# Kernel tuning notes

Hardware: AMD Instinct MI355X
Metric: run time of the kernel (lower is better)

The kernel has to match this reference:

```python
import jax, jax.numpy as jnp
import numpy as np

N_HEAD = 12
N_TILES = 10  # forward hardcodes t = T // 10 and repeats the tril mask 10x10


def setup_inputs() -> dict:
    key = jax.random.key(0)
    ks = jax.random.split(key, 9)
    B, T, C = 2, 2560, 768
    s = 1.0 / np.sqrt(C)
    x = jax.random.normal(ks[0], (B, T, C), dtype=jnp.float32)
    Wk = jax.random.normal(ks[1], (C, C), dtype=jnp.float32) * s
    bk = jnp.zeros((C,), dtype=jnp.float32)
    Wq = jax.random.normal(ks[2], (C, C), dtype=jnp.float32) * s
    bq = jnp.zeros((C,), dtype=jnp.float32)
    Wv = jax.random.normal(ks[3], (C, C), dtype=jnp.float32) * s
    bv = jnp.zeros((C,), dtype=jnp.float32)
    Wp = jax.random.normal(ks[4], (C, C), dtype=jnp.float32) * s
    bp = jnp.zeros((C,), dtype=jnp.float32)
    return {"x": x, "Wk": Wk, "bk": bk, "Wq": Wq, "bq": bq,
            "Wv": Wv, "bv": bv, "Wp": Wp, "bp": bp}


def reference(x, Wk, bk, Wq, bq, Wv, bv, Wp, bp):
    B, T, C = x.shape
    hd = C // N_HEAD
    t = T // N_TILES
    # linear projections (torch nn.Linear: x @ W.T + b)
    k = (x @ Wk.T + bk).reshape(B, T, N_HEAD, hd).transpose(0, 2, 1, 3)  # [B,H,T,hd]
    q = (x @ Wq.T + bq).reshape(B, T, N_HEAD, hd).transpose(0, 2, 1, 3)
    v = (x @ Wv.T + bv).reshape(B, T, N_HEAD, hd).transpose(0, 2, 1, 3)
    att = jnp.einsum('bhqd,bhkd->bhqk', q, k) * (1.0 / np.sqrt(hd))  # [B,H,T,T]
    # repeated block-tril mask: tril(t,t) tiled 10x10 over TxT
    idx = jnp.arange(T)
    mask = (idx[:, None] % t) >= (idx[None, :] % t)  # [T,T] bool
    att = jnp.where(mask[None, None], att, -jnp.inf)
    att = jax.nn.softmax(att, axis=-1)
    y = jnp.einsum('bhqk,bhkd->bhqd', att, v)  # [B,H,T,hd]
    y = y.transpose(0, 2, 1, 3).reshape(B, T, C)
    return y @ Wp.T + bp
```

## Files before the change

### kernel.cpp

```cpp
#include <hip/hip_runtime.h>

typedef unsigned short u16;
typedef unsigned int u32;
typedef __bf16 bf16x8 __attribute__((ext_vector_type(8)));
typedef short s16x4 __attribute__((ext_vector_type(4)));
typedef float f32x4 __attribute__((ext_vector_type(4)));

#define CC 768
#define TT 2560
#define NH 12
#define HD 64
#define KDIM 768

#define QSCALE 0.18033688011112042f

__device__ __forceinline__ u16 f2bf(float f) {
  u32 u = __builtin_bit_cast(u32, f);
  u32 r = u + 0x7fffu + ((u >> 16) & 1u);
  return (u16)(r >> 16);
}

#if __has_builtin(__builtin_amdgcn_mfma_f32_16x16x16bf16_1k)
__device__ __forceinline__ f32x4 mfma16b(s16x4 a, s16x4 b, f32x4 c) {
  return __builtin_amdgcn_mfma_f32_16x16x16bf16_1k(a, b, c, 0, 0, 0);
}
#else
__device__ __forceinline__ f32x4 mfma16b(s16x4 a, s16x4 b, f32x4 c) {
  f32x4 d;
  asm("v_mfma_f32_16x16x16_bf16 %0, %1, %2, %3\n\ts_nop 7\n\ts_nop 7"
      : "=v"(d) : "v"(a), "v"(b), "v"(c));
  return d;
}
#endif

__global__ void convall(const float* __restrict__ x,
                        const float* __restrict__ Wq, const float* __restrict__ Wk,
                        const float* __restrict__ Wv, const float* __restrict__ Wp,
                        u16* __restrict__ xb, u16* __restrict__ wqb, u16* __restrict__ wkb,
                        u16* __restrict__ wvb, u16* __restrict__ wpb,
                        int nx4, int nw4) {
  int z = blockIdx.y;
  const float* in; u16* out; int n4;
  switch (z) {
    case 0: in = x;  out = xb;  n4 = nx4; break;
    case 1: in = Wq; out = wqb; n4 = nw4; break;
    case 2: in = Wk; out = wkb; n4 = nw4; break;
    case 3: in = Wv; out = wvb; n4 = nw4; break;
    default: in = Wp; out = wpb; n4 = nw4; break;
  }
  int i = blockIdx.x * blockDim.x + threadIdx.x;
  if (i >= n4) return;
  float4 v = ((const float4*)in)[i];
  ushort4 o;
  o.x = f2bf(v.x); o.y = f2bf(v.y); o.z = f2bf(v.z); o.w = f2bf(v.w);
  ((ushort4*)out)[i] = o;
}

__global__ __launch_bounds__(256) void gemm_qkv(
    const u16* __restrict__ xb,
    const u16* __restrict__ wqb, const u16* __restrict__ wkb, const u16* __restrict__ wvb,
    const float* __restrict__ bq, const float* __restrict__ bk, const float* __restrict__ bv,
    u16* __restrict__ qo, u16* __restrict__ ko, u16* __restrict__ vo)
{
  __shared__ __align__(16) u16 lds_a[128 * 72];
  __shared__ __align__(16) u16 lds_b[128 * 72];
  int z = blockIdx.z;
  const u16* W = (z == 0) ? wqb : (z == 1 ? wkb : wvb);
  const float* bias = (z == 0) ? bq : (z == 1 ? bk : bv);
  int n0 = blockIdx.x * 128;
  int m0 = blockIdx.y * 128;
  int tid = threadIdx.x;
  int lane = tid & 63, wv_ = tid >> 6;
  int wm = wv_ & 1, wn = wv_ >> 1;
  int mcol = lane & 15, quad = lane >> 4;
  int chunk = tid & 7, rbase = tid >> 3;

  f32x4 acc[4][4] = {};

  for (int k0 = 0; k0 < KDIM; k0 += 64) {
    __syncthreads();
#pragma unroll
    for (int r = 0; r < 4; ++r) {
      int row = rbase + r * 32;
      *(uint4*)&lds_a[row * 72 + chunk * 8] =
          *(const uint4*)&xb[(size_t)(m0 + row) * KDIM + k0 + chunk * 8];
      *(uint4*)&lds_b[row * 72 + chunk * 8] =
          *(const uint4*)&W[(size_t)(n0 + row) * KDIM + k0 + chunk * 8];
    }
    __syncthreads();
#pragma unroll
    for (int kc = 0; kc < 2; ++kc) {
      bf16x8 af[4], bfr[4];
#pragma unroll
      for (int i = 0; i < 4; i++)
        af[i] = *(const bf16x8*)&lds_a[(wm * 64 + i * 16 + mcol) * 72 + kc * 32 + quad * 8];
#pragma unroll
      for (int i = 0; i < 4; i++)
        bfr[i] = *(const bf16x8*)&lds_b[(wn * 64 + i * 16 + mcol) * 72 + kc * 32 + quad * 8];
      if (z == 2) {
#pragma unroll
        for (int i = 0; i < 4; i++)
#pragma unroll
          for (int j = 0; j < 4; j++)
            acc[i][j] = __builtin_amdgcn_mfma_f32_16x16x32_bf16(af[i], bfr[j], acc[i][j], 0, 0, 0);
      } else {
#pragma unroll
        for (int i = 0; i < 4; i++)
#pragma unroll
          for (int j = 0; j < 4; j++)
            acc[i][j] = __builtin_amdgcn_mfma_f32_16x16x32_bf16(bfr[j], af[i], acc[i][j], 0, 0, 0);
      }
    }
  }

  if (z == 2) {
#pragma unroll
    for (int i = 0; i < 4; i++) {
      int rowb = m0 + wm * 64 + i * 16 + quad * 4;
      int b = rowb / TT;
      int tt0 = rowb - b * TT;
#pragma unroll
      for (int j = 0; j < 4; j++) {
        int col = n0 + wn * 64 + j * 16 + mcol;
        int h = col >> 6, d = col & 63;
        float bb_ = bias[col];
        size_t bhoff = (size_t)(b * NH + h) * (TT * HD);
        ushort4 pk;
        pk.x = f2bf(acc[i][j][0] + bb_);
        pk.y = f2bf(acc[i][j][1] + bb_);
        pk.z = f2bf(acc[i][j][2] + bb_);
        pk.w = f2bf(acc[i][j][3] + bb_);
        *(ushort4*)&vo[bhoff + (size_t)(tt0 >> 4) * 1024 + d * 16 + (tt0 & 15)] = pk;
      }
    }
  } else {
    u16* dst = (z == 0) ? qo : ko;
    float scale = (z == 0) ? QSCALE : 1.0f;
#pragma unroll
    for (int i = 0; i < 4; i++) {
      int token = m0 + wm * 64 + i * 16 + mcol;
      int b = token / TT;
      int tt = token - b * TT;
#pragma unroll
      for (int j = 0; j < 4; j++) {
        int ch0 = n0 + wn * 64 + j * 16 + quad * 4;
        int h = ch0 >> 6, d4 = ch0 & 63;
        float4 bb4 = *(const float4*)&bias[ch0];
        size_t bhoff = (size_t)(b * NH + h) * (TT * HD);
        ushort4 pk;
        pk.x = f2bf((acc[i][j][0] + bb4.x) * scale);
        pk.y = f2bf((acc[i][j][1] + bb4.y) * scale);
        pk.z = f2bf((acc[i][j][2] + bb4.z) * scale);
        pk.w = f2bf((acc[i][j][3] + bb4.w) * scale);
        if (z == 0) {
          *(ushort4*)&dst[bhoff + (size_t)tt * HD + d4] = pk;
        } else {
          *(ushort4*)&dst[bhoff + (size_t)(tt >> 4) * 1024 + (d4 >> 5) * 512 +
                          (tt & 15) * 32 + (d4 & 31)] = pk;
        }
      }
    }
  }
}

struct Strip {
  bf16x8 qf0, qf1;
  f32x4 o0, o1, o2, o3;
  f32x4 racc;
};

__device__ __forceinline__ void strip_step(
    Strip& S, bf16x8 kf0, bf16x8 kf1,
    s16x4 vf0, s16x4 vf1, s16x4 vf2, s16x4 vf3,
    bool maskg, int mcol, int quad)
{
  f32x4 st = {0.f, 0.f, 0.f, 0.f};
  st = __builtin_amdgcn_mfma_f32_16x16x32_bf16(kf0, S.qf0, st, 0, 0, 0);
  st = __builtin_amdgcn_mfma_f32_16x16x32_bf16(kf1, S.qf1, st, 0, 0, 0);
  float p0 = __builtin_amdgcn_exp2f(st[0]);
  float p1 = __builtin_amdgcn_exp2f(st[1]);
  float p2 = __builtin_amdgcn_exp2f(st[2]);
  float p3 = __builtin_amdgcn_exp2f(st[3]);
  if (maskg) {
    int j0 = quad * 4;
    p0 = (j0 + 0 > mcol) ? 0.f : p0;
    p1 = (j0 + 1 > mcol) ? 0.f : p1;
    p2 = (j0 + 2 > mcol) ? 0.f : p2;
    p3 = (j0 + 3 > mcol) ? 0.f : p3;
  }
  uint2 pk;
  pk.x = __builtin_amdgcn_perm(__builtin_bit_cast(u32, p1),
                               __builtin_bit_cast(u32, p0), 0x07060302u);
  pk.y = __builtin_amdgcn_perm(__builtin_bit_cast(u32, p3),
                               __builtin_bit_cast(u32, p2), 0x07060302u);
  s16x4 pf = __builtin_bit_cast(s16x4, pk);
  const s16x4 ones = {0x3F80, 0x3F80, 0x3F80, 0x3F80};
  S.racc = mfma16b(ones, pf, S.racc);
  S.o0 = mfma16b(vf0, pf, S.o0);
  S.o1 = mfma16b(vf1, pf, S.o1);
  S.o2 = mfma16b(vf2, pf, S.o2);
  S.o3 = mfma16b(vf3, pf, S.o3);
}

#define OSTR 68

__global__ __launch_bounds__(128) void attn(
    const u16* __restrict__ q, const u16* __restrict__ kg,
    const u16* __restrict__ vg, u16* __restrict__ y)
{
  __shared__ float lds_o[4][16 * OSTR];
  __shared__ float lds_r[64];

  int tid = threadIdx.x;
  int lane = tid & 63, w = tid >> 6;
  int mcol = lane & 15, quad = lane >> 4;
  int gid = blockIdx.x;
  int c = gid & 7;
  int idx = gid >> 3;
  int sub = idx / 40;
  int s = idx - sub * 40;
  int bh = c * 3 + sub;
  int hb = s >> 3;
  int r = s & 7;
  int b = bh / NH, h = bh - b * NH;
  const u16* qp = q + (size_t)bh * TT * HD;
  const u16* kp = kg + (size_t)bh * TT * HD;
  const u16* vp = vg + (size_t)bh * TT * HD;

  int base = hb * 512;
  int rh = 7 - r;
  int qr[4];
  qr[0] = base + r * 16;
  qr[1] = base + 128 + rh * 16;
  qr[2] = base + 256 + r * 16;
  qr[3] = base + 384 + rh * 16;

  Strip S[4];
#pragma unroll
  for (int i = 0; i < 4; ++i) {
    S[i].qf0 = *(const bf16x8*)&qp[(size_t)(qr[i] + mcol) * HD + quad * 8];
    S[i].qf1 = *(const bf16x8*)&qp[(size_t)(qr[i] + mcol) * HD + 32 + quad * 8];
    S[i].o0 = {0.f, 0.f, 0.f, 0.f};
    S[i].o1 = {0.f, 0.f, 0.f, 0.f};
    S[i].o2 = {0.f, 0.f, 0.f, 0.f};
    S[i].o3 = {0.f, 0.f, 0.f, 0.f};
    S[i].racc = {0.f, 0.f, 0.f, 0.f};
  }

  int koff = mcol * 32 + quad * 8;
  int voff = mcol * 16 + quad * 4;

  for (int kt = w * 10; kt < w * 10 + 10; ++kt) {
    const u16* ktb = kp + kt * (128 * HD);
    const u16* vtb = vp + kt * (128 * HD);
    if ((kt & 1) == 0) {
#pragma unroll
      for (int g = 0; g < 8; ++g) {
        bf16x8 kf0 = *(const bf16x8*)&ktb[g * 1024 + koff];
        bf16x8 kf1 = *(const bf16x8*)&ktb[g * 1024 + 512 + koff];
        s16x4 vf0 = *(const s16x4*)&vtb[g * 1024 + 0 * 256 + voff];
        s16x4 vf1 = *(const s16x4*)&vtb[g * 1024 + 1 * 256 + voff];
        s16x4 vf2 = *(const s16x4*)&vtb[g * 1024 + 2 * 256 + voff];
        s16x4 vf3 = *(const s16x4*)&vtb[g * 1024 + 3 * 256 + voff];
        strip_step(S[1], kf0, kf1, vf0, vf1, vf2, vf3, false, mcol, quad);
        strip_step(S[3], kf0, kf1, vf0, vf1, vf2, vf3, false, mcol, quad);
        if (g <= r) {
          bool mg = (g == r);
          strip_step(S[0], kf0, kf1, vf0, vf1, vf2, vf3, mg, mcol, quad);
          strip_step(S[2], kf0, kf1, vf0, vf1, vf2, vf3, mg, mcol, quad);
        }
      }
    } else {
      for (int g = 0; g <= rh; ++g) {
        bf16x8 kf0 = *(const bf16x8*)&ktb[g * 1024 + koff];
        bf16x8 kf1 = *(const bf16x8*)&ktb[g * 1024 + 512 + koff];
        s16x4 vf0 = *(const s16x4*)&vtb[g * 1024 + 0 * 256 + voff];
        s16x4 vf1 = *(const s16x4*)&vtb[g * 1024 + 1 * 256 + voff];
        s16x4 vf2 = *(const s16x4*)&vtb[g * 1024 + 2 * 256 + voff];
        s16x4 vf3 = *(const s16x4*)&vtb[g * 1024 + 3 * 256 + voff];
        bool mg = (g == rh);
        strip_step(S[1], kf0, kf1, vf0, vf1, vf2, vf3, mg, mcol, quad);
        strip_step(S[3], kf0, kf1, vf0, vf1, vf2, vf3, mg, mcol, quad);
      }
    }
  }

  if (w == 1) {
#pragma unroll
    for (int i = 0; i < 4; ++i) {
      f32x4 oo[4] = {S[i].o0, S[i].o1, S[i].o2, S[i].o3};
#pragma unroll
      for (int df = 0; df < 4; ++df)
        *(f32x4*)&lds_o[i][mcol * OSTR + df * 16 + quad * 4] = oo[df];
      if (quad == 0) lds_r[i * 16 + mcol] = S[i].racc[0];
    }
  }
  __syncthreads();
  if (w == 0) {
#pragma unroll
    for (int i = 0; i < 4; ++i) {
      float denom = S[i].racc[0] + lds_r[i * 16 + mcol];
      float inv = 1.0f / denom;
      f32x4 oo[4] = {S[i].o0, S[i].o1, S[i].o2, S[i].o3};
      size_t yrow = ((size_t)(b * TT + qr[i] + mcol)) * CC + h * HD;
#pragma unroll
      for (int df = 0; df < 4; ++df) {
        f32x4 other = *(const f32x4*)&lds_o[i][mcol * OSTR + df * 16 + quad * 4];
        ushort4 pk;
        pk.x = f2bf((oo[df][0] + other[0]) * inv);
        pk.y = f2bf((oo[df][1] + other[1]) * inv);
        pk.z = f2bf((oo[df][2] + other[2]) * inv);
        pk.w = f2bf((oo[df][3] + other[3]) * inv);
        *(ushort4*)&y[yrow + df * 16 + quad * 4] = pk;
      }
    }
  }
}

__global__ __launch_bounds__(256) void gemm_out(
    const u16* __restrict__ yb, const u16* __restrict__ wpb,
    const float* __restrict__ bp, float* __restrict__ out)
{
  __shared__ __align__(16) u16 lds_a[64 * 72];
  __shared__ __align__(16) u16 lds_b[128 * 72];
  int n0 = blockIdx.x * 128;
  int m0 = blockIdx.y * 64;
  int tid = threadIdx.x;
  int lane = tid & 63, wv_ = tid >> 6;
  int wm = wv_ & 1, wn = wv_ >> 1;
  int mcol = lane & 15, quad = lane >> 4;
  int chunk = tid & 7, rbase = tid >> 3;

  f32x4 acc[2][4] = {};

  for (int k0 = 0; k0 < KDIM; k0 += 64) {
    __syncthreads();
#pragma unroll
    for (int r = 0; r < 2; ++r) {
      int row = rbase + r * 32;
      *(uint4*)&lds_a[row * 72 + chunk * 8] =
          *(const uint4*)&yb[(size_t)(m0 + row) * KDIM + k0 + chunk * 8];
    }
#pragma unroll
    for (int r = 0; r < 4; ++r) {
      int row = rbase + r * 32;
      *(uint4*)&lds_b[row * 72 + chunk * 8] =
          *(const uint4*)&wpb[(size_t)(n0 + row) * KDIM + k0 + chunk * 8];
    }
    __syncthreads();
#pragma unroll
    for (int kc = 0; kc < 2; ++kc) {
      bf16x8 af[2], bfr[4];
#pragma unroll
      for (int i = 0; i < 2; i++)
        af[i] = *(const bf16x8*)&lds_a[(wm * 32 + i * 16 + mcol) * 72 + kc * 32 + quad * 8];
#pragma unroll
      for (int j = 0; j < 4; j++)
        bfr[j] = *(const bf16x8*)&lds_b[(wn * 64 + j * 16 + mcol) * 72 + kc * 32 + quad * 8];
#pragma unroll
      for (int i = 0; i < 2; i++)
#pragma unroll
        for (int j = 0; j < 4; j++)
          acc[i][j] = __builtin_amdgcn_mfma_f32_16x16x32_bf16(bfr[j], af[i], acc[i][j], 0, 0, 0);
    }
  }

#pragma unroll
  for (int i = 0; i < 2; i++) {
    int token = m0 + wm * 32 + i * 16 + mcol;
#pragma unroll
    for (int j = 0; j < 4; j++) {
      int ch0 = n0 + wn * 64 + j * 16 + quad * 4;
      float4 bb4 = *(const float4*)&bp[ch0];
      float4 o4;
      o4.x = acc[i][j][0] + bb4.x;
      o4.y = acc[i][j][1] + bb4.y;
      o4.z = acc[i][j][2] + bb4.z;
      o4.w = acc[i][j][3] + bb4.w;
      *(float4*)&out[(size_t)token * CC + ch0] = o4;
    }
  }
}

extern "C" void kernel_launch(void* const* d_in, const int* in_sizes, int n_in,
                              void* d_out, int out_size, void* d_ws, size_t ws_size,
                              hipStream_t stream) {
  const float* x  = (const float*)d_in[0];
  const float* Wk = (const float*)d_in[1];
  const float* bk = (const float*)d_in[2];
  const float* Wq = (const float*)d_in[3];
  const float* bq = (const float*)d_in[4];
  const float* Wv = (const float*)d_in[5];
  const float* bv = (const float*)d_in[6];
  const float* Wp = (const float*)d_in[7];
  const float* bp = (const float*)d_in[8];
  float* out = (float*)d_out;

  char* ws = (char*)d_ws;
  size_t off = 0;
  auto alloc = [&](size_t bytes) {
    void* p = ws + off;
    off += (bytes + 255) & ~(size_t)255;
    return p;
  };
  const size_t NX = (size_t)2 * TT * CC;
  const size_t NW = (size_t)CC * CC;
  u16* xb  = (u16*)alloc(NX * 2);
  u16* wqb = (u16*)alloc(NW * 2);
  u16* wkb = (u16*)alloc(NW * 2);
  u16* wvb = (u16*)alloc(NW * 2);
  u16* wpb = (u16*)alloc(NW * 2);
  u16* qws = (u16*)alloc(NX * 2);
  u16* kws = (u16*)alloc(NX * 2);
  u16* vgw = (u16*)alloc(NX * 2);
  u16* yws = (u16*)alloc(NX * 2);

  int nx4 = (int)(NX / 4), nw4 = (int)(NW / 4);
  convall<<<dim3((nx4 + 255) / 256, 5), 256, 0, stream>>>(
      x, Wq, Wk, Wv, Wp, xb, wqb, wkb, wvb, wpb, nx4, nw4);

  gemm_qkv<<<dim3(6, 40, 3), 256, 0, stream>>>(xb, wqb, wkb, wvb, bq, bk, bv,
                                               qws, kws, vgw);
  attn<<<dim3(960), 128, 0, stream>>>(qws, kws, vgw, yws);
  gemm_out<<<dim3(6, 80), 256, 0, stream>>>(yws, wpb, bp, out);
}
```

Measured before the change: 188.9 us.

## Split attention key tiles across four waves with tree reduction

New measurement: 194.4 us. +2.9%, slower.

```diff
diff --git a/kernel.cpp b/kernel.cpp
--- a/kernel.cpp
+++ b/kernel.cpp
@@ -204,12 +204,12 @@
 
 #define OSTR 68
 
-__global__ __launch_bounds__(128) void attn(
+__global__ __launch_bounds__(256) void attn(
     const u16* __restrict__ q, const u16* __restrict__ kg,
     const u16* __restrict__ vg, u16* __restrict__ y)
 {
-  __shared__ float lds_o[4][16 * OSTR];
-  __shared__ float lds_r[64];
+  __shared__ float lds_o[2][4][16 * OSTR];
+  __shared__ float lds_r[2][64];
 
   int tid = threadIdx.x;
   int lane = tid & 63, w = tid >> 6;
@@ -250,7 +250,7 @@
   int koff = mcol * 32 + quad * 8;
   int voff = mcol * 16 + quad * 4;
 
-  for (int kt = w * 10; kt < w * 10 + 10; ++kt) {
+  for (int kt = w * 5; kt < w * 5 + 5; ++kt) {
     const u16* ktb = kp + kt * (128 * HD);
     const u16* vtb = vp + kt * (128 * HD);
     if ((kt & 1) == 0) {
@@ -285,35 +285,60 @@
     }
   }
 
-  if (w == 1) {
-#pragma unroll
-    for (int i = 0; i < 4; ++i) {
-      f32x4 oo[4] = {S[i].o0, S[i].o1, S[i].o2, S[i].o3};
-#pragma unroll
-      for (int df = 0; df < 4; ++df)
-        *(f32x4*)&lds_o[i][mcol * OSTR + df * 16 + quad * 4] = oo[df];
-      if (quad == 0) lds_r[i * 16 + mcol] = S[i].racc[0];
-    }
+  auto spillb = [&](const Strip& Si, int bi, int i) {
+    f32x4 oo[4] = {Si.o0, Si.o1, Si.o2, Si.o3};
+#pragma unroll
+    for (int df = 0; df < 4; ++df)
+      *(f32x4*)&lds_o[bi][i][mcol * OSTR + df * 16 + quad * 4] = oo[df];
+    if (quad == 0) lds_r[bi][i * 16 + mcol] = Si.racc[0];
+  };
+  auto gatherb = [&](Strip& Si, int bi, int i) {
+    f32x4 t0 = *(const f32x4*)&lds_o[bi][i][mcol * OSTR + 0 * 16 + quad * 4];
+    f32x4 t1 = *(const f32x4*)&lds_o[bi][i][mcol * OSTR + 1 * 16 + quad * 4];
+    f32x4 t2 = *(const f32x4*)&lds_o[bi][i][mcol * OSTR + 2 * 16 + quad * 4];
+    f32x4 t3 = *(const f32x4*)&lds_o[bi][i][mcol * OSTR + 3 * 16 + quad * 4];
+    Si.o0 += t0; Si.o1 += t1; Si.o2 += t2; Si.o3 += t3;
+    Si.racc[0] += lds_r[bi][i * 16 + mcol];
+  };
+  auto finish = [&](const Strip& Si, int i, int qrow) {
+    float denom = Si.racc[0] + lds_r[0][i * 16 + mcol];
+    float inv = 1.0f / denom;
+    f32x4 oo[4] = {Si.o0, Si.o1, Si.o2, Si.o3};
+    size_t yrow = ((size_t)(b * TT + qrow + mcol)) * CC + h * HD;
+#pragma unroll
+    for (int df = 0; df < 4; ++df) {
+      f32x4 other = *(const f32x4*)&lds_o[0][i][mcol * OSTR + df * 16 + quad * 4];
+      ushort4 pk;
+      pk.x = f2bf((oo[df][0] + other[0]) * inv);
+      pk.y = f2bf((oo[df][1] + other[1]) * inv);
+      pk.z = f2bf((oo[df][2] + other[2]) * inv);
+      pk.w = f2bf((oo[df][3] + other[3]) * inv);
+      *(ushort4*)&y[yrow + df * 16 + quad * 4] = pk;
+    }
+  };
+
+  if (w & 1) {
+    int bi = w >> 1;
+    spillb(S[0], bi, 0); spillb(S[1], bi, 1);
+    spillb(S[2], bi, 2); spillb(S[3], bi, 3);
+  }
+  __syncthreads();
+  if (!(w & 1)) {
+    int bi = w >> 1;
+    gatherb(S[0], bi, 0); gatherb(S[1], bi, 1);
+    gatherb(S[2], bi, 2); gatherb(S[3], bi, 3);
   }
   __syncthreads();
   if (w == 0) {
-#pragma unroll
-    for (int i = 0; i < 4; ++i) {
-      float denom = S[i].racc[0] + lds_r[i * 16 + mcol];
-      float inv = 1.0f / denom;
-      f32x4 oo[4] = {S[i].o0, S[i].o1, S[i].o2, S[i].o3};
-      size_t yrow = ((size_t)(b * TT + qr[i] + mcol)) * CC + h * HD;
-#pragma unroll
-      for (int df = 0; df < 4; ++df) {
-        f32x4 other = *(const f32x4*)&lds_o[i][mcol * OSTR + df * 16 + quad * 4];
-        ushort4 pk;
-        pk.x = f2bf((oo[df][0] + other[0]) * inv);
-        pk.y = f2bf((oo[df][1] + other[1]) * inv);
-        pk.z = f2bf((oo[df][2] + other[2]) * inv);
-        pk.w = f2bf((oo[df][3] + other[3]) * inv);
-        *(ushort4*)&y[yrow + df * 16 + quad * 4] = pk;
-      }
-    }
+    spillb(S[2], 0, 2); spillb(S[3], 0, 3);
+  } else if (w == 2) {
+    spillb(S[0], 0, 0); spillb(S[1], 0, 1);
+  }
+  __syncthreads();
+  if (w == 0) {
+    finish(S[0], 0, qr[0]); finish(S[1], 1, qr[1]);
+  } else if (w == 2) {
+    finish(S[2], 2, qr[2]); finish(S[3], 3, qr[3]);
   }
 }
 
@@ -421,6 +446,6 @@
 
   gemm_qkv<<<dim3(6, 40, 3), 256, 0, stream>>>(xb, wqb, wkb, wvb, bq, bk, bv,
                                                qws, kws, vgw);
-  attn<<<dim3(960), 128, 0, stream>>>(qws, kws, vgw, yws);
+  attn<<<dim3(960), 256, 0, stream>>>(qws, kws, vgw, yws);
   gemm_out<<<dim3(6, 80), 256, 0, stream>>>(yws, wpb, bp, out);
 }
```

## Split attention key range across five waves with LDS Q slab and atomic reduction

Applied to the files above, without the earlier changes.

After: 319.7 us. 1.69x slower.

```diff
diff --git a/kernel.cpp b/kernel.cpp
--- a/kernel.cpp
+++ b/kernel.cpp
@@ -163,20 +163,24 @@
   }
 }
 
-struct Strip {
-  bf16x8 qf0, qf1;
+struct StripS {
   f32x4 o0, o1, o2, o3;
-  f32x4 racc;
+  float rs;
+  int qb;
 };
 
 __device__ __forceinline__ void strip_step(
-    Strip& S, bf16x8 kf0, bf16x8 kf1,
+    StripS& S, const u16* qsl, bf16x8 kf0, bf16x8 kf1,
     s16x4 vf0, s16x4 vf1, s16x4 vf2, s16x4 vf3,
     bool maskg, int mcol, int quad)
 {
+  int qo = S.qb;
+  asm volatile("" : "+v"(qo));
+  bf16x8 qf0 = *(const bf16x8*)&qsl[qo];
+  bf16x8 qf1 = *(const bf16x8*)&qsl[qo ^ 32];
   f32x4 st = {0.f, 0.f, 0.f, 0.f};
-  st = __builtin_amdgcn_mfma_f32_16x16x32_bf16(kf0, S.qf0, st, 0, 0, 0);
-  st = __builtin_amdgcn_mfma_f32_16x16x32_bf16(kf1, S.qf1, st, 0, 0, 0);
+  st = __builtin_amdgcn_mfma_f32_16x16x32_bf16(kf0, qf0, st, 0, 0, 0);
+  st = __builtin_amdgcn_mfma_f32_16x16x32_bf16(kf1, qf1, st, 0, 0, 0);
   float p0 = __builtin_amdgcn_exp2f(st[0]);
   float p1 = __builtin_amdgcn_exp2f(st[1]);
   float p2 = __builtin_amdgcn_exp2f(st[2]);
@@ -188,28 +192,32 @@
     p2 = (j0 + 2 > mcol) ? 0.f : p2;
     p3 = (j0 + 3 > mcol) ? 0.f : p3;
   }
+  u32 t0 = __builtin_bit_cast(u32, p0) & 0xffff0000u;
+  u32 t1 = __builtin_bit_cast(u32, p1) & 0xffff0000u;
+  u32 t2 = __builtin_bit_cast(u32, p2) & 0xffff0000u;
+  u32 t3 = __builtin_bit_cast(u32, p3) & 0xffff0000u;
+  S.rs += (__builtin_bit_cast(float, t0) + __builtin_bit_cast(float, t1)) +
+          (__builtin_bit_cast(float, t2) + __builtin_bit_cast(float, t3));
   uint2 pk;
-  pk.x = __builtin_amdgcn_perm(__builtin_bit_cast(u32, p1),
-                               __builtin_bit_cast(u32, p0), 0x07060302u);
-  pk.y = __builtin_amdgcn_perm(__builtin_bit_cast(u32, p3),
-                               __builtin_bit_cast(u32, p2), 0x07060302u);
+  pk.x = __builtin_amdgcn_perm(t1, t0, 0x07060302u);
+  pk.y = __builtin_amdgcn_perm(t3, t2, 0x07060302u);
   s16x4 pf = __builtin_bit_cast(s16x4, pk);
-  const s16x4 ones = {0x3F80, 0x3F80, 0x3F80, 0x3F80};
-  S.racc = mfma16b(ones, pf, S.racc);
   S.o0 = mfma16b(vf0, pf, S.o0);
   S.o1 = mfma16b(vf1, pf, S.o1);
   S.o2 = mfma16b(vf2, pf, S.o2);
   S.o3 = mfma16b(vf3, pf, S.o3);
 }
 
-#define OSTR 68
-
-__global__ __launch_bounds__(128) void attn(
+#define CSTR 65
+
+__global__ __launch_bounds__(320, 3) void attn(
     const u16* __restrict__ q, const u16* __restrict__ kg,
     const u16* __restrict__ vg, u16* __restrict__ y)
 {
-  __shared__ float lds_o[4][16 * OSTR];
-  __shared__ float lds_r[64];
+  __shared__ __align__(16) char lds_raw[(4 * 16 * CSTR + 4 * 16) * 4];
+  u16* qslab = (u16*)lds_raw;
+  float (*lds_c)[16][CSTR] = (float (*)[16][CSTR])lds_raw;
+  float* lds_d = (float*)(lds_raw + 4 * 16 * CSTR * 4);
 
   int tid = threadIdx.x;
   int lane = tid & 63, w = tid >> 6;
@@ -235,22 +243,30 @@
   qr[2] = base + 256 + r * 16;
   qr[3] = base + 384 + rh * 16;
 
-  Strip S[4];
+  for (int i = tid; i < 512; i += 320) {
+    int s_ = i >> 7, rw = (i >> 3) & 15, cc = i & 7;
+    uint4 v = *(const uint4*)&qp[(size_t)(qr[s_] + rw) * HD + cc * 8];
+    *(uint4*)&qslab[((s_ * 16 + rw) * 8 + (cc ^ (rw & 7))) * 8] = v;
+  }
+  __syncthreads();
+
+  int qc0 = (quad ^ (mcol & 7)) * 8;
+
+  StripS S[4];
 #pragma unroll
   for (int i = 0; i < 4; ++i) {
-    S[i].qf0 = *(const bf16x8*)&qp[(size_t)(qr[i] + mcol) * HD + quad * 8];
-    S[i].qf1 = *(const bf16x8*)&qp[(size_t)(qr[i] + mcol) * HD + 32 + quad * 8];
     S[i].o0 = {0.f, 0.f, 0.f, 0.f};
     S[i].o1 = {0.f, 0.f, 0.f, 0.f};
     S[i].o2 = {0.f, 0.f, 0.f, 0.f};
     S[i].o3 = {0.f, 0.f, 0.f, 0.f};
-    S[i].racc = {0.f, 0.f, 0.f, 0.f};
+    S[i].rs = 0.f;
+    S[i].qb = (i * 16 + mcol) * 64 + qc0;
   }
 
   int koff = mcol * 32 + quad * 8;
   int voff = mcol * 16 + quad * 4;
 
-  for (int kt = w * 10; kt < w * 10 + 10; ++kt) {
+  for (int kt = w * 4; kt < w * 4 + 4; ++kt) {
     const u16* ktb = kp + kt * (128 * HD);
     const u16* vtb = vp + kt * (128 * HD);
     if ((kt & 1) == 0) {
@@ -262,12 +278,12 @@
         s16x4 vf1 = *(const s16x4*)&vtb[g * 1024 + 1 * 256 + voff];
         s16x4 vf2 = *(const s16x4*)&vtb[g * 1024 + 2 * 256 + voff];
         s16x4 vf3 = *(const s16x4*)&vtb[g * 1024 + 3 * 256 + voff];
-        strip_step(S[1], kf0, kf1, vf0, vf1, vf2, vf3, false, mcol, quad);
-        strip_step(S[3], kf0, kf1, vf0, vf1, vf2, vf3, false, mcol, quad);
+        strip_step(S[1], qslab, kf0, kf1, vf0, vf1, vf2, vf3, false, mcol, quad);
+        strip_step(S[3], qslab, kf0, kf1, vf0, vf1, vf2, vf3, false, mcol, quad);
         if (g <= r) {
           bool mg = (g == r);
-          strip_step(S[0], kf0, kf1, vf0, vf1, vf2, vf3, mg, mcol, quad);
-          strip_step(S[2], kf0, kf1, vf0, vf1, vf2, vf3, mg, mcol, quad);
+          strip_step(S[0], qslab, kf0, kf1, vf0, vf1, vf2, vf3, mg, mcol, quad);
+          strip_step(S[2], qslab, kf0, kf1, vf0, vf1, vf2, vf3, mg, mcol, quad);
         }
       }
     } else {
@@ -279,40 +295,52 @@
         s16x4 vf2 = *(const s16x4*)&vtb[g * 1024 + 2 * 256 + voff];
         s16x4 vf3 = *(const s16x4*)&vtb[g * 1024 + 3 * 256 + voff];
         bool mg = (g == rh);
-        strip_step(S[1], kf0, kf1, vf0, vf1, vf2, vf3, mg, mcol, quad);
-        strip_step(S[3], kf0, kf1, vf0, vf1, vf2, vf3, mg, mcol, quad);
+        strip_step(S[1], qslab, kf0, kf1, vf0, vf1, vf2, vf3, mg, mcol, quad);
+        strip_step(S[3], qslab, kf0, kf1, vf0, vf1, vf2, vf3, mg, mcol, quad);
       }
     }
   }
 
-  if (w == 1) {
-#pragma unroll
-    for (int i = 0; i < 4; ++i) {
-      f32x4 oo[4] = {S[i].o0, S[i].o1, S[i].o2, S[i].o3};
-#pragma unroll
-      for (int df = 0; df < 4; ++df)
-        *(f32x4*)&lds_o[i][mcol * OSTR + df * 16 + quad * 4] = oo[df];
-      if (quad == 0) lds_r[i * 16 + mcol] = S[i].racc[0];
-    }
-  }
+#pragma unroll
+  for (int i = 0; i < 4; ++i) {
+    float r_ = S[i].rs;
+    r_ += __shfl_xor(r_, 16);
+    r_ += __shfl_xor(r_, 32);
+    S[i].rs = r_;
+  }
+
   __syncthreads();
-  if (w == 0) {
-#pragma unroll
-    for (int i = 0; i < 4; ++i) {
-      float denom = S[i].racc[0] + lds_r[i * 16 + mcol];
-      float inv = 1.0f / denom;
-      f32x4 oo[4] = {S[i].o0, S[i].o1, S[i].o2, S[i].o3};
-      size_t yrow = ((size_t)(b * TT + qr[i] + mcol)) * CC + h * HD;
-#pragma unroll
-      for (int df = 0; df < 4; ++df) {
-        f32x4 other = *(const f32x4*)&lds_o[i][mcol * OSTR + df * 16 + quad * 4];
-        ushort4 pk;
-        pk.x = f2bf((oo[df][0] + other[0]) * inv);
-        pk.y = f2bf((oo[df][1] + other[1]) * inv);
-        pk.z = f2bf((oo[df][2] + other[2]) * inv);
-        pk.w = f2bf((oo[df][3] + other[3]) * inv);
-        *(ushort4*)&y[yrow + df * 16 + quad * 4] = pk;
-      }
+  {
+    float* cflat = (float*)lds_raw;
+    for (int i = tid; i < 4 * 16 * CSTR + 4 * 16; i += 320) cflat[i] = 0.f;
+  }
+  __syncthreads();
+#pragma unroll
+  for (int i = 0; i < 4; ++i) {
+    float* cb = &lds_c[i][mcol][0];
+    f32x4 oo[4] = {S[i].o0, S[i].o1, S[i].o2, S[i].o3};
+#pragma unroll
+    for (int df = 0; df < 4; ++df)
+#pragma unroll
+      for (int e = 0; e < 4; ++e)
+        atomicAdd(&cb[df * 16 + quad * 4 + e], oo[df][e]);
+    if (quad == 0) atomicAdd(&lds_d[i * 16 + mcol], S[i].rs);
+  }
+  __syncthreads();
+  if (w < 4) {
+    int i = w;
+    float inv = 1.0f / lds_d[i * 16 + mcol];
+    const float* cb = &lds_c[i][mcol][0];
+    size_t yrow = ((size_t)(b * TT + qr[i] + mcol)) * CC + h * HD;
+#pragma unroll
+    for (int df = 0; df < 4; ++df) {
+      int c0 = df * 16 + quad * 4;
+      ushort4 pk;
+      pk.x = f2bf(cb[c0 + 0] * inv);
+      pk.y = f2bf(cb[c0 + 1] * inv);
+      pk.z = f2bf(cb[c0 + 2] * inv);
+      pk.w = f2bf(cb[c0 + 3] * inv);
+      *(ushort4*)&y[yrow + c0] = pk;
     }
   }
 }
@@ -421,6 +449,6 @@
 
   gemm_qkv<<<dim3(6, 40, 3), 256, 0, stream>>>(xb, wqb, wkb, wvb, bq, bk, bv,
                                                qws, kws, vgw);
-  attn<<<dim3(960), 128, 0, stream>>>(qws, kws, vgw, yws);
+  attn<<<dim3(960), 320, 0, stream>>>(qws, kws, vgw, yws);
   gemm_out<<<dim3(6, 80), 256, 0, stream>>>(yws, wpb, bp, out);
 }
```

## Fuse fp32-to-bf16 conversion into GEMM loads and prefetch K/V fragments in attention

Applied to the files above, without the earlier changes.

After: 212.4 us. 12.5% more time.

```diff
diff --git a/kernel.cpp b/kernel.cpp
--- a/kernel.cpp
+++ b/kernel.cpp
@@ -18,6 +18,17 @@
   u32 u = __builtin_bit_cast(u32, f);
   u32 r = u + 0x7fffu + ((u >> 16) & 1u);
   return (u16)(r >> 16);
+}
+
+__device__ __forceinline__ uint4 cvt8(const float* p) {
+  float4 a = *(const float4*)p;
+  float4 b = *(const float4*)(p + 4);
+  uint4 o;
+  o.x = ((u32)f2bf(a.y) << 16) | f2bf(a.x);
+  o.y = ((u32)f2bf(a.w) << 16) | f2bf(a.z);
+  o.z = ((u32)f2bf(b.y) << 16) | f2bf(b.x);
+  o.w = ((u32)f2bf(b.w) << 16) | f2bf(b.z);
+  return o;
 }
 
 #if __has_builtin(__builtin_amdgcn_mfma_f32_16x16x16bf16_1k)
@@ -33,39 +44,18 @@
 }
 #endif
 
-__global__ void convall(const float* __restrict__ x,
-                        const float* __restrict__ Wq, const float* __restrict__ Wk,
-                        const float* __restrict__ Wv, const float* __restrict__ Wp,
-                        u16* __restrict__ xb, u16* __restrict__ wqb, u16* __restrict__ wkb,
-                        u16* __restrict__ wvb, u16* __restrict__ wpb,
-                        int nx4, int nw4) {
-  int z = blockIdx.y;
-  const float* in; u16* out; int n4;
-  switch (z) {
-    case 0: in = x;  out = xb;  n4 = nx4; break;
-    case 1: in = Wq; out = wqb; n4 = nw4; break;
-    case 2: in = Wk; out = wkb; n4 = nw4; break;
-    case 3: in = Wv; out = wvb; n4 = nw4; break;
-    default: in = Wp; out = wpb; n4 = nw4; break;
-  }
-  int i = blockIdx.x * blockDim.x + threadIdx.x;
-  if (i >= n4) return;
-  float4 v = ((const float4*)in)[i];
-  ushort4 o;
-  o.x = f2bf(v.x); o.y = f2bf(v.y); o.z = f2bf(v.z); o.w = f2bf(v.w);
-  ((ushort4*)out)[i] = o;
-}
-
 __global__ __launch_bounds__(256) void gemm_qkv(
-    const u16* __restrict__ xb,
-    const u16* __restrict__ wqb, const u16* __restrict__ wkb, const u16* __restrict__ wvb,
-    const float* __restrict__ bq, const float* __restrict__ bk, const float* __restrict__ bv,
+    const float* __restrict__ x,
+    const float* __restrict__ Wq, const float* __restrict__ Wk,
+    const float* __restrict__ Wv,
+    const float* __restrict__ bq, const float* __restrict__ bk,
+    const float* __restrict__ bv,
     u16* __restrict__ qo, u16* __restrict__ ko, u16* __restrict__ vo)
 {
   __shared__ __align__(16) u16 lds_a[128 * 72];
   __shared__ __align__(16) u16 lds_b[128 * 72];
   int z = blockIdx.z;
-  const u16* W = (z == 0) ? wqb : (z == 1 ? wkb : wvb);
+  const float* W = (z == 0) ? Wq : (z == 1 ? Wk : Wv);
   const float* bias = (z == 0) ? bq : (z == 1 ? bk : bv);
   int n0 = blockIdx.x * 128;
   int m0 = blockIdx.y * 128;
@@ -83,9 +73,9 @@
     for (int r = 0; r < 4; ++r) {
       int row = rbase + r * 32;
       *(uint4*)&lds_a[row * 72 + chunk * 8] =
-          *(const uint4*)&xb[(size_t)(m0 + row) * KDIM + k0 + chunk * 8];
+          cvt8(&x[(size_t)(m0 + row) * KDIM + k0 + chunk * 8]);
       *(uint4*)&lds_b[row * 72 + chunk * 8] =
-          *(const uint4*)&W[(size_t)(n0 + row) * KDIM + k0 + chunk * 8];
+          cvt8(&W[(size_t)(n0 + row) * KDIM + k0 + chunk * 8]);
     }
     __syncthreads();
 #pragma unroll
@@ -254,14 +244,25 @@
     const u16* ktb = kp + kt * (128 * HD);
     const u16* vtb = vp + kt * (128 * HD);
     if ((kt & 1) == 0) {
+      bf16x8 kf0 = *(const bf16x8*)&ktb[koff];
+      bf16x8 kf1 = *(const bf16x8*)&ktb[512 + koff];
+      s16x4 vf0 = *(const s16x4*)&vtb[0 * 256 + voff];
+      s16x4 vf1 = *(const s16x4*)&vtb[1 * 256 + voff];
+      s16x4 vf2 = *(const s16x4*)&vtb[2 * 256 + voff];
+      s16x4 vf3 = *(const s16x4*)&vtb[3 * 256 + voff];
 #pragma unroll
       for (int g = 0; g < 8; ++g) {
-        bf16x8 kf0 = *(const bf16x8*)&ktb[g * 1024 + koff];
-        bf16x8 kf1 = *(const bf16x8*)&ktb[g * 1024 + 512 + koff];
-        s16x4 vf0 = *(const s16x4*)&vtb[g * 1024 + 0 * 256 + voff];
-        s16x4 vf1 = *(const s16x4*)&vtb[g * 1024 + 1 * 256 + voff];
-        s16x4 vf2 = *(const s16x4*)&vtb[g * 1024 + 2 * 256 + voff];
-        s16x4 vf3 = *(const s16x4*)&vtb[g * 1024 + 3 * 256 + voff];
+        bf16x8 nk0, nk1; s16x4 nv0, nv1, nv2, nv3;
+        if (g < 7) {
+          const u16* kn = ktb + (g + 1) * 1024;
+          const u16* vn = vtb + (g + 1) * 1024;
+          nk0 = *(const bf16x8*)&kn[koff];
+          nk1 = *(const bf16x8*)&kn[512 + koff];
+          nv0 = *(const s16x4*)&vn[0 * 256 + voff];
+          nv1 = *(const s16x4*)&vn[1 * 256 + voff];
+          nv2 = *(const s16x4*)&vn[2 * 256 + voff];
+          nv3 = *(const s16x4*)&vn[3 * 256 + voff];
+        }
         strip_step(S[1], kf0, kf1, vf0, vf1, vf2, vf3, false, mcol, quad);
         strip_step(S[3], kf0, kf1, vf0, vf1, vf2, vf3, false, mcol, quad);
         if (g <= r) {
@@ -269,18 +270,33 @@
           strip_step(S[0], kf0, kf1, vf0, vf1, vf2, vf3, mg, mcol, quad);
           strip_step(S[2], kf0, kf1, vf0, vf1, vf2, vf3, mg, mcol, quad);
         }
+        if (g < 7) {
+          kf0 = nk0; kf1 = nk1;
+          vf0 = nv0; vf1 = nv1; vf2 = nv2; vf3 = nv3;
+        }
       }
     } else {
+      bf16x8 kf0 = *(const bf16x8*)&ktb[koff];
+      bf16x8 kf1 = *(const bf16x8*)&ktb[512 + koff];
+      s16x4 vf0 = *(const s16x4*)&vtb[0 * 256 + voff];
+      s16x4 vf1 = *(const s16x4*)&vtb[1 * 256 + voff];
+      s16x4 vf2 = *(const s16x4*)&vtb[2 * 256 + voff];
+      s16x4 vf3 = *(const s16x4*)&vtb[3 * 256 + voff];
       for (int g = 0; g <= rh; ++g) {
-        bf16x8 kf0 = *(const bf16x8*)&ktb[g * 1024 + koff];
-        bf16x8 kf1 = *(const bf16x8*)&ktb[g * 1024 + 512 + koff];
-        s16x4 vf0 = *(const s16x4*)&vtb[g * 1024 + 0 * 256 + voff];
-        s16x4 vf1 = *(const s16x4*)&vtb[g * 1024 + 1 * 256 + voff];
-        s16x4 vf2 = *(const s16x4*)&vtb[g * 1024 + 2 * 256 + voff];
-        s16x4 vf3 = *(const s16x4*)&vtb[g * 1024 + 3 * 256 + voff];
+        int gn = (g < rh) ? g + 1 : g;
+        const u16* kn = ktb + gn * 1024;
+        const u16* vn = vtb + gn * 1024;
+        bf16x8 nk0 = *(const bf16x8*)&kn[koff];
+        bf16x8 nk1 = *(const bf16x8*)&kn[512 + koff];
+        s16x4 nv0 = *(const s16x4*)&vn[0 * 256 + voff];
+        s16x4 nv1 = *(const s16x4*)&vn[1 * 256 + voff];
+        s16x4 nv2 = *(const s16x4*)&vn[2 * 256 + voff];
+        s16x4 nv3 = *(const s16x4*)&vn[3 * 256 + voff];
         bool mg = (g == rh);
         strip_step(S[1], kf0, kf1, vf0, vf1, vf2, vf3, mg, mcol, quad);
         strip_step(S[3], kf0, kf1, vf0, vf1, vf2, vf3, mg, mcol, quad);
+        kf0 = nk0; kf1 = nk1;
+        vf0 = nv0; vf1 = nv1; vf2 = nv2; vf3 = nv3;
       }
     }
   }
@@ -318,7 +334,7 @@
 }
 
 __global__ __launch_bounds__(256) void gemm_out(
-    const u16* __restrict__ yb, const u16* __restrict__ wpb,
+    const u16* __restrict__ yb, const float* __restrict__ Wp,
     const float* __restrict__ bp, float* __restrict__ out)
 {
   __shared__ __align__(16) u16 lds_a[64 * 72];
@@ -345,7 +361,7 @@
     for (int r = 0; r < 4; ++r) {
       int row = rbase + r * 32;
       *(uint4*)&lds_b[row * 72 + chunk * 8] =
-          *(const uint4*)&wpb[(size_t)(n0 + row) * KDIM + k0 + chunk * 8];
+          cvt8(&Wp[(size_t)(n0 + row) * KDIM + k0 + chunk * 8]);
     }
     __syncthreads();
 #pragma unroll
@@ -404,23 +420,13 @@
     return p;
   };
   const size_t NX = (size_t)2 * TT * CC;
-  const size_t NW = (size_t)CC * CC;
-  u16* xb  = (u16*)alloc(NX * 2);
-  u16* wqb = (u16*)alloc(NW * 2);
-  u16* wkb = (u16*)alloc(NW * 2);
-  u16* wvb = (u16*)alloc(NW * 2);
-  u16* wpb = (u16*)alloc(NW * 2);
   u16* qws = (u16*)alloc(NX * 2);
   u16* kws = (u16*)alloc(NX * 2);
   u16* vgw = (u16*)alloc(NX * 2);
   u16* yws = (u16*)alloc(NX * 2);
 
-  int nx4 = (int)(NX / 4), nw4 = (int)(NW / 4);
-  convall<<<dim3((nx4 + 255) / 256, 5), 256, 0, stream>>>(
-      x, Wq, Wk, Wv, Wp, xb, wqb, wkb, wvb, wpb, nx4, nw4);
-
-  gemm_qkv<<<dim3(6, 40, 3), 256, 0, stream>>>(xb, wqb, wkb, wvb, bq, bk, bv,
+  gemm_qkv<<<dim3(6, 40, 3), 256, 0, stream>>>(x, Wq, Wk, Wv, bq, bk, bv,
                                                qws, kws, vgw);
   attn<<<dim3(960), 128, 0, stream>>>(qws, kws, vgw, yws);
-  gemm_out<<<dim3(6, 80), 256, 0, stream>>>(yws, wpb, bp, out);
-}
+  gemm_out<<<dim3(6, 80), 256, 0, stream>>>(yws, Wp, bp, out);
+}
```
